# Kernel optimization log

Measured on AMD Instinct MI355X. Metric: run time of the kernel, lower is better.

Reference implementation:

```python
import jax, jax.numpy as jnp
import numpy as np

N = 50000   # nodes
E = 400000  # edges
R = 35      # num_relations
B = 12      # num_bases
C = 128     # hidden_conv_dim (heads=1)
T = 4       # node types: load, gen, load_gen, ext
HL = 38     # hidden_lin_dim
OUT = 2


def setup_inputs() -> dict:
    key = jax.random.key(0)
    ks = jax.random.split(key, 24)
    s = 0.1  # param scale
    inp = {
        'x': jax.random.normal(ks[0], (N, 2), jnp.float32),
        'edge_index': jax.random.randint(ks[1], (2, E), 0, N, jnp.int32),
        'edge_type': jax.random.randint(ks[2], (E,), 0, R, jnp.int32),
        'edge_attr': jax.random.normal(ks[3], (E, 2), jnp.float32),
        'node_type': jax.random.randint(ks[4], (N,), 0, T, jnp.int32),
        'basis': jax.random.normal(ks[5], (B, 2, C), jnp.float32) * s,
        'att_rel': jax.random.normal(ks[6], (R, B), jnp.float32) * s,
        'q_att': jax.random.normal(ks[7], (C, 1), jnp.float32) * s,
        'k_att': jax.random.normal(ks[8], (C, 1), jnp.float32) * s,
        'e_att': jax.random.normal(ks[9], (C, 1), jnp.float32) * s,
        'lin_edge_W': jax.random.normal(ks[10], (2, C), jnp.float32) * s,
        'conv_bias': jax.random.normal(ks[11], (C,), jnp.float32) * s,
        'lin0_W': jax.random.normal(ks[12], (T, C, HL), jnp.float32) * s,
        'lin0_b': jax.random.normal(ks[13], (T, HL), jnp.float32) * s,
        'lin1_W': jax.random.normal(ks[14], (T, HL, HL), jnp.float32) * s,
        'lin1_b': jax.random.normal(ks[15], (T, HL), jnp.float32) * s,
        'lin2_W': jax.random.normal(ks[16], (T, HL, HL), jnp.float32) * s,
        'lin2_b': jax.random.normal(ks[17], (T, HL), jnp.float32) * s,
        'fin_W': jax.random.normal(ks[18], (T, HL, OUT), jnp.float32) * s,
        'fin_b': jax.random.normal(ks[19], (T, OUT), jnp.float32) * s,
    }
    return inp


def _segment_softmax(alpha, dst, n):
    # PyG softmax: max is detached, eps=1e-16 on the denominator
    amax = jax.lax.stop_gradient(jax.ops.segment_max(alpha, dst, num_segments=n))
    ex = jnp.exp(alpha - amax[dst])
    den = jax.ops.segment_sum(ex, dst, num_segments=n) + 1e-16
    return ex / den[dst]


def _per_type_linear(xv, W, b, t):
    # apply node-type-specific Linear: [N,d] x [T,d,h] -> pick row type
    y = jnp.einsum('nd,tdh->nth', xv, W)              # [N,T,h]
    y = jnp.take_along_axis(y, t[:, None, None], axis=1)[:, 0]
    return y + b[t]


def reference(x, edge_index, edge_type, edge_attr, node_type,
              basis, att_rel, q_att, k_att, e_att, lin_edge_W, conv_bias,
              lin0_W, lin0_b, lin1_W, lin1_b, lin2_W, lin2_b, fin_W, fin_b):
    n = x.shape[0]
    src, dst = edge_index[0], edge_index[1]
    # RGATConv with basis decomposition: per-relation weight [R, in=2, C]
    w = jnp.einsum('rb,bio->rio', att_rel, basis)
    w_e = w[edge_type]                                 # [E,2,C] edge gather
    out_i = jnp.einsum('ei,eic->ec', x[dst], w_e)      # [E,C]
    out_j = jnp.einsum('ei,eic->ec', x[src], w_e)      # [E,C]
    ke = (edge_attr @ lin_edge_W) @ e_att              # [E,1]
    alpha = out_i @ q_att + out_j @ k_att + ke         # additive self-attention
    alpha = jax.nn.leaky_relu(alpha, 0.2)
    alpha = _segment_softmax(alpha, dst, n)            # across-relation segment softmax
    msg = alpha * out_j                                # heads=1 -> [E,C]
    agg = jax.ops.segment_sum(msg, dst, num_segments=n) + conv_bias
    h = jax.nn.leaky_relu(agg, 0.2)                    # forward activation (dropout: eval)
    t = node_type
    h = _per_type_linear(jax.nn.relu(h), lin0_W, lin0_b, t)
    h = _per_type_linear(jax.nn.relu(h), lin1_W, lin1_b, t)
    h = _per_type_linear(jax.nn.relu(h), lin2_W, lin2_b, t)
    out = _per_type_linear(h, fin_W, fin_b, t)         # [N,2]
    # load nodes (type 0): second output passes through abs
    load_out = jnp.concatenate([out[:, :1], jnp.abs(out[:, 1:2])], axis=1)
    return jnp.where((t == 0)[:, None], load_out, out)
```

## Files before the change

kernel.cpp:

```cpp
#include <hip/hip_runtime.h>
#include <math.h>

#define N_NODES 50000
#define N_EDGES 400000
#define R_REL   35
#define B_BASES 12
#define C_DIM   128
#define HL_DIM  38
#define RI2     70
#define NP      50304
#define NB_HIST 196
#define NBUCK   786
#define EPB     2048
#define CAP     704

#define OFF_WT     0
#define OFF_WQ     8960
#define OFF_WK     9030
#define OFF_LE     9100
#define OFF_META   9104
#define OFF_HBLK   9120
#define OFF_BBASE  9904
#define OFF_PERM   10688
#define OFF_INV    60688
#define OFF_ECUR   110992
#define OFF_EREC   111780

#define CH    0
#define ST    3584
#define HH    8344
#define Y2T   11608
#define SM_DINV 16536
#define SM_CB   16600
#define SM_B0   16728
#define SM_B1   16766
#define SM_B2   16804
#define SM_FW   16844
#define SM_FB   16920
#define LDS_FLOATS 16928

__global__ __launch_bounds__(256) void k_init(const int* __restrict__ node_type,
                                              const float* __restrict__ basis,
                                              const float* __restrict__ att_rel,
                                              float* __restrict__ ws) {
    int b = blockIdx.x, tid = threadIdx.x;
    if (b < NB_HIST) {
        __shared__ int lh[4];
        if (tid < 4) lh[tid] = 0;
        __syncthreads();
        int i = b * 256 + tid;
        if (i < N_NODES) atomicAdd(&lh[node_type[i]], 1);
        __syncthreads();
        if (tid < 4) ((int*)(ws + OFF_HBLK))[b * 4 + tid] = lh[tid];
    } else if (b < NB_HIST + 35) {
        int idx = (b - NB_HIST) * 256 + tid;
        if (idx < RI2 * C_DIM) {
            int c  = idx & (C_DIM - 1);
            int ri = idx >> 7;
            int r = ri >> 1, ii = ri & 1;
            float acc = 0.f;
            #pragma unroll
            for (int bb = 0; bb < B_BASES; ++bb)
                acc += att_rel[r * B_BASES + bb] * basis[(bb * 2 + ii) * C_DIM + c];
            ws[OFF_WT + idx] = acc;
        }
    } else {
        for (int i = tid; i < NBUCK; i += 256) ((int*)(ws + OFF_ECUR))[i] = 0;
    }
}

__global__ __launch_bounds__(256) void k_scanproj(const float* __restrict__ q_att,
                                                  const float* __restrict__ k_att,
                                                  const float* __restrict__ e_att,
                                                  const float* __restrict__ lin_edge_W,
                                                  float* __restrict__ ws) {
    int b = blockIdx.x, tid = threadIdx.x;
    int lane = tid & 63, wv = tid >> 6;
    if (b == 0) {
        __shared__ int lh[NB_HIST * 4];
        __shared__ int basel[4];
        const int* hblk = (const int*)(ws + OFF_HBLK);
        for (int i = tid; i < NB_HIST * 4; i += 256) lh[i] = hblk[i];
        __syncthreads();
        __shared__ int tot[4];
        if (tid < 4) {
            int run = 0;
            for (int bb = 0; bb < NB_HIST; ++bb) {
                int v = lh[bb * 4 + tid];
                lh[bb * 4 + tid] = run;
                run += v;
            }
            tot[tid] = run;
        }
        __syncthreads();
        if (tid == 0) {
            int* meta = (int*)(ws + OFF_META);
            int t0 = tot[0], t1 = tot[1], t2 = tot[2], t3 = tot[3];
            int b1 = ((t0 + 63) >> 6) << 6;
            int b2 = b1 + (((t1 + 63) >> 6) << 6);
            int b3 = b2 + (((t2 + 63) >> 6) << 6);
            meta[0] = t0; meta[1] = t1; meta[2] = t2; meta[3] = t3;
            meta[4] = 0;  meta[5] = b1; meta[6] = b2; meta[7] = b3;
            basel[0] = 0; basel[1] = b1; basel[2] = b2; basel[3] = b3;
        }
        __syncthreads();
        for (int i = tid; i < NB_HIST * 4; i += 256)
            ((int*)(ws + OFF_BBASE))[i] = basel[i & 3] + lh[i];
    } else {
        int u = (b - 1) * 4 + wv;
        if (u < RI2) {
            const float* wr = ws + OFF_WT + u * C_DIM;
            float w1 = wr[lane], w2 = wr[64 + lane];
            float aq = w1 * q_att[lane] + w2 * q_att[64 + lane];
            float ak = w1 * k_att[lane] + w2 * k_att[64 + lane];
            #pragma unroll
            for (int off = 32; off; off >>= 1) {
                aq += __shfl_xor(aq, off, 64);
                ak += __shfl_xor(ak, off, 64);
            }
            if (lane == 0) { ws[OFF_WQ + u] = aq; ws[OFF_WK + u] = ak; }
        } else if (u < 72) {
            int j = u - RI2;
            const float* er = lin_edge_W + j * C_DIM;
            float a = er[lane] * e_att[lane] + er[64 + lane] * e_att[64 + lane];
            #pragma unroll
            for (int off = 32; off; off >>= 1) a += __shfl_xor(a, off, 64);
            if (lane == 0) ws[OFF_LE + j] = a;
        }
    }
}

__global__ __launch_bounds__(256) void k_perm(const int* __restrict__ node_type,
                                              float* __restrict__ ws) {
    __shared__ int wcnt[4][4];
    int tid = threadIdx.x;
    int lane = tid & 63, wv = tid >> 6;
    int n = blockIdx.x * 256 + tid;
    bool active = n < N_NODES;
    int ty = active ? node_type[n] : -1;
    int myrank = 0;
    #pragma unroll
    for (int t = 0; t < 4; ++t) {
        unsigned long long m = __ballot(ty == t);
        if (lane == 0) wcnt[wv][t] = __popcll(m);
        if (ty == t) myrank = __popcll(m & ((1ULL << lane) - 1ULL));
    }
    __syncthreads();
    if (active) {
        int pre = 0;
        for (int w2 = 0; w2 < wv; ++w2) pre += wcnt[w2][ty];
        int p = ((const int*)(ws + OFF_BBASE))[blockIdx.x * 4 + ty] + pre + myrank;
        ((int*)(ws + OFF_PERM))[n] = p;
        ((int*)(ws + OFF_INV))[p] = n;
    }
}

__global__ __launch_bounds__(256) void k_escatter(const float* __restrict__ x,
                                                  const int* __restrict__ edge_index,
                                                  const int* __restrict__ edge_type,
                                                  const float* __restrict__ edge_attr,
                                                  float* __restrict__ ws) {
    __shared__ int hist[NBUCK];
    __shared__ int sbase[NBUCK];
    __shared__ float swq[RI2], swk[RI2], sle[2];
    int tid = threadIdx.x;
    for (int i = tid; i < NBUCK; i += 256) hist[i] = 0;
    if (tid < RI2) { swq[tid] = ws[OFF_WQ + tid]; swk[tid] = ws[OFF_WK + tid]; }
    if (tid < 2) sle[tid] = ws[OFF_LE + tid];
    __syncthreads();

    const int* perm = (const int*)(ws + OFF_PERM);
    int base = blockIdx.x * EPB;
    int   rb[8], rm[8];
    float rex[8], rsx[8], rsy[8];
    #pragma unroll
    for (int k = 0; k < 8; ++k) {
        int e = base + k * 256 + tid;
        rb[k] = -1;
        if (e < N_EDGES) {
            int src = edge_index[e];
            int dst = edge_index[N_EDGES + e];
            int r   = edge_type[e];
            int p   = perm[dst];
            float2 ea = *(const float2*)(edge_attr + 2 * e);
            float2 xs = *(const float2*)(x + 2 * src);
            float2 xd = *(const float2*)(x + 2 * dst);
            float alpha = xd.x * swq[2 * r] + xd.y * swq[2 * r + 1]
                        + xs.x * swk[2 * r] + xs.y * swk[2 * r + 1]
                        + ea.x * sle[0]     + ea.y * sle[1];
            alpha = alpha > 0.f ? alpha : 0.2f * alpha;
            float ex = __expf(alpha);
            rb[k]  = p >> 6;
            rm[k]  = (r << 6) | (p & 63);
            rex[k] = ex;
            rsx[k] = ex * xs.x;
            rsy[k] = ex * xs.y;
            atomicAdd(&hist[rb[k]], 1);
        }
    }
    __syncthreads();
    int* gcur = (int*)(ws + OFF_ECUR);
    for (int i = tid; i < NBUCK; i += 256) {
        int c = hist[i];
        sbase[i] = (c > 0) ? atomicAdd(&gcur[i], c) : 0;
    }
    __syncthreads();
    float4* rec = (float4*)(ws + OFF_EREC);
    #pragma unroll
    for (int k = 0; k < 8; ++k) {
        if (rb[k] >= 0) {
            int slot = atomicAdd(&sbase[rb[k]], 1);
            rec[(size_t)rb[k] * CAP + slot] =
                make_float4(__int_as_float(rm[k]), rex[k], rsx[k], rsy[k]);
        }
    }
}

__global__ __launch_bounds__(256) void k_node(
        const float* __restrict__ ws, const float* __restrict__ conv_bias,
        const float* __restrict__ lin0_W, const float* __restrict__ lin0_b,
        const float* __restrict__ lin1_W, const float* __restrict__ lin1_b,
        const float* __restrict__ lin2_W, const float* __restrict__ lin2_b,
        const float* __restrict__ fin_W,  const float* __restrict__ fin_b,
        float* __restrict__ out) {
    __shared__ float L[LDS_FLOATS];
    int tid  = threadIdx.x;
    int lane = tid & 63;
    int wv   = tid >> 6;
    int p0   = blockIdx.x * 64;

    const int* meta = (const int*)(ws + OFF_META);
    int b1 = meta[5], b2 = meta[6], b3 = meta[7];
    int t  = (p0 >= b1) + (p0 >= b2) + (p0 >= b3);
    int bp = meta[4 + t];
    int cnt = meta[t];

    for (int i = tid; i < RI2 * 68; i += 256) L[ST + i] = 0.f;
    if (tid < 64) L[SM_DINV + tid] = 0.f;
    if (tid < 128) L[SM_CB + tid] = conv_bias[tid];
    if (tid >= 64 && tid < 256) {
        int i = tid - 64;
        if      (i < 38)  L[SM_B0 + i]        = lin0_b[t * HL_DIM + i];
        else if (i < 76)  L[SM_B1 + i - 38]   = lin1_b[t * HL_DIM + i - 38];
        else if (i < 114) L[SM_B2 + i - 76]   = lin2_b[t * HL_DIM + i - 76];
        else if (i < 190) L[SM_FW + i - 114]  = fin_W[t * 76 + i - 114];
        else              L[SM_FB + i - 190]  = fin_b[t * 2 + i - 190];
    }
    const float* wT_g = ws + OFF_WT;
    for (int i4 = tid; i4 < 448; i4 += 256) {
        float4 v = ((const float4*)wT_g)[i4];
        *(float4*)&L[CH + i4 * 4] = v;
    }
    __syncthreads();

    {
        int ecnt = ((const int*)(ws + OFF_ECUR))[blockIdx.x];
        const float4* rec = (const float4*)(ws + OFF_EREC) + (size_t)blockIdx.x * CAP;
        for (int i = tid; i < ecnt; i += 256) {
            float4 v = rec[i];
            int m = __float_as_int(v.x);
            int n = m & 63, r = m >> 6;
            atomicAdd(&L[ST + (2 * r) * 68 + n],     v.z);
            atomicAdd(&L[ST + (2 * r + 1) * 68 + n], v.w);
            atomicAdd(&L[SM_DINV + n],               v.y);
        }
    }
    __syncthreads();
    if (tid < 64) L[SM_DINV + tid] = 1.0f / (L[SM_DINV + tid] + 1e-16f);

    int ng = lane & 15, cg_ = lane >> 4;
    int c0 = wv * 32 + cg_ * 8;
    float acc[32];
    #pragma unroll
    for (int i = 0; i < 32; ++i) acc[i] = 0.f;
    int cur = 0;
    for (int q = 0; q < 5; ++q) {
        float4 pf0, pf1;
        if (q < 4) {
            const float4* src = (const float4*)(wT_g + (q + 1) * 1792);
            pf0 = src[tid];
            if (tid < 192) pf1 = src[tid + 256];
        }
        const float* wb = &L[CH + cur * 1792];
        #pragma unroll
        for (int kk = 0; kk < 14; ++kk) {
            float4 a4 = *(const float4*)&L[ST + (q * 14 + kk) * 68 + ng * 4];
            float4 wa = *(const float4*)&wb[kk * 128 + c0];
            float4 wc = *(const float4*)&wb[kk * 128 + c0 + 4];
            float a_[4] = {a4.x, a4.y, a4.z, a4.w};
            float w_[8] = {wa.x, wa.y, wa.z, wa.w, wc.x, wc.y, wc.z, wc.w};
            #pragma unroll
            for (int ni = 0; ni < 4; ++ni)
                #pragma unroll
                for (int ci = 0; ci < 8; ++ci)
                    acc[ni * 8 + ci] += a_[ni] * w_[ci];
        }
        if (q < 4) {
            float* dstb = &L[CH + (cur ^ 1) * 1792];
            *(float4*)&dstb[tid * 4] = pf0;
            if (tid < 192) *(float4*)&dstb[(tid + 256) * 4] = pf1;
        }
        cur ^= 1;
        __syncthreads();
    }

    {
        float4 dv = *(const float4*)&L[SM_DINV + ng * 4];
        float d_[4] = {dv.x, dv.y, dv.z, dv.w};
        #pragma unroll
        for (int ci = 0; ci < 8; ++ci) {
            float cb = L[SM_CB + c0 + ci];
            float4 hv;
            float h0 = acc[0 * 8 + ci] * d_[0] + cb;
            float h1 = acc[1 * 8 + ci] * d_[1] + cb;
            float h2 = acc[2 * 8 + ci] * d_[2] + cb;
            float h3 = acc[3 * 8 + ci] * d_[3] + cb;
            hv.x = h0 > 0.f ? h0 : 0.f;
            hv.y = h1 > 0.f ? h1 : 0.f;
            hv.z = h2 > 0.f ? h2 : 0.f;
            hv.w = h3 > 0.f ? h3 : 0.f;
            *(float4*)&L[HH + (c0 + ci) * 64 + ng * 4] = hv;
        }
    }
    const float* W0g = lin0_W + t * C_DIM * HL_DIM;
    for (int i = tid; i < 608; i += 256) {
        int cc = i / 38, j = i - cc * 38;
        L[CH + cc * 40 + j] = W0g[i];
    }
    __syncthreads();

    int jg = lane >> 4;
    int j0 = wv * 16 + jg * 4;
    float acc2[16];
    #pragma unroll
    for (int i = 0; i < 16; ++i) acc2[i] = 0.f;
    int cur2 = 0;
    for (int q = 0; q < 8; ++q) {
        float pa, pb, pc;
        if (q < 7) {
            const float* src = W0g + (q + 1) * 608;
            pa = src[tid];
            if (tid < 608 - 256) pb = src[tid + 256];
            if (tid < 608 - 512) pc = src[tid + 512];
        }
        const float* wb = &L[CH + cur2 * 1792];
        #pragma unroll
        for (int kk = 0; kk < 16; ++kk) {
            int c = q * 16 + kk;
            float4 a4 = *(const float4*)&L[HH + c * 64 + ng * 4];
            float4 w4 = *(const float4*)&wb[kk * 40 + j0];
            float a_[4] = {a4.x, a4.y, a4.z, a4.w};
            float w_[4] = {w4.x, w4.y, w4.z, w4.w};
            #pragma unroll
            for (int ni = 0; ni < 4; ++ni)
                #pragma unroll
                for (int ji = 0; ji < 4; ++ji)
                    acc2[ni * 4 + ji] += a_[ni] * w_[ji];
        }
        if (q < 7) {
            float* dstb = &L[CH + (cur2 ^ 1) * 1792];
            int i = tid, cc = i / 38, j = i - cc * 38;
            dstb[cc * 40 + j] = pa;
            if (tid < 608 - 256) { i = tid + 256; cc = i / 38; j = i - cc * 38; dstb[cc * 40 + j] = pb; }
            if (tid < 608 - 512) { i = tid + 512; cc = i / 38; j = i - cc * 38; dstb[cc * 40 + j] = pc; }
        }
        cur2 ^= 1;
        __syncthreads();
    }
    #pragma unroll
    for (int ji = 0; ji < 4; ++ji) {
        int j = j0 + ji;
        float b = (j < 38) ? L[SM_B0 + j] : 0.f;
        float4 yv;
        float y0 = acc2[0 * 4 + ji] + b;
        float y1 = acc2[1 * 4 + ji] + b;
        float y2 = acc2[2 * 4 + ji] + b;
        float y3 = acc2[3 * 4 + ji] + b;
        yv.x = y0 > 0.f ? y0 : 0.f;
        yv.y = y1 > 0.f ? y1 : 0.f;
        yv.z = y2 > 0.f ? y2 : 0.f;
        yv.w = y3 > 0.f ? y3 : 0.f;
        *(float4*)&L[ST + j * 68 + ng * 4] = yv;
    }
    {
        const float* W1g = lin1_W + t * HL_DIM * HL_DIM;
        const float* W2g = lin2_W + t * HL_DIM * HL_DIM;
        for (int i = tid; i < 1444; i += 256) {
            int cc = i / 38, j = i - cc * 38;
            L[CH + cc * 40 + j] = W1g[i];
            L[CH + 1520 + cc * 40 + j] = W2g[i];
        }
    }
    __syncthreads();

    float acc3[16];
    #pragma unroll
    for (int i = 0; i < 16; ++i) acc3[i] = 0.f;
    #pragma unroll 2
    for (int kk = 0; kk < 38; ++kk) {
        float4 a4 = *(const float4*)&L[ST + kk * 68 + ng * 4];
        float4 w4 = *(const float4*)&L[CH + kk * 40 + j0];
        float a_[4] = {a4.x, a4.y, a4.z, a4.w};
        float w_[4] = {w4.x, w4.y, w4.z, w4.w};
        #pragma unroll
        for (int ni = 0; ni < 4; ++ni)
            #pragma unroll
            for (int ji = 0; ji < 4; ++ji)
                acc3[ni * 4 + ji] += a_[ni] * w_[ji];
    }
    __syncthreads();
    #pragma unroll
    for (int ji = 0; ji < 4; ++ji) {
        int j = j0 + ji;
        float b = (j < 38) ? L[SM_B1 + j] : 0.f;
        float4 yv;
        float y0 = acc3[0 * 4 + ji] + b;
        float y1 = acc3[1 * 4 + ji] + b;
        float y2 = acc3[2 * 4 + ji] + b;
        float y3 = acc3[3 * 4 + ji] + b;
        yv.x = y0 > 0.f ? y0 : 0.f;
        yv.y = y1 > 0.f ? y1 : 0.f;
        yv.z = y2 > 0.f ? y2 : 0.f;
        yv.w = y3 > 0.f ? y3 : 0.f;
        *(float4*)&L[HH + j * 68 + ng * 4] = yv;
    }
    __syncthreads();

    float acc4[16];
    #pragma unroll
    for (int i = 0; i < 16; ++i) acc4[i] = 0.f;
    #pragma unroll 2
    for (int kk = 0; kk < 38; ++kk) {
        float4 a4 = *(const float4*)&L[HH + kk * 68 + ng * 4];
        float4 w4 = *(const float4*)&L[CH + 1520 + kk * 40 + j0];
        float a_[4] = {a4.x, a4.y, a4.z, a4.w};
        float w_[4] = {w4.x, w4.y, w4.z, w4.w};
        #pragma unroll
        for (int ni = 0; ni < 4; ++ni)
            #pragma unroll
            for (int ji = 0; ji < 4; ++ji)
                acc4[ni * 4 + ji] += a_[ni] * w_[ji];
    }
    #pragma unroll
    for (int ji = 0; ji < 4; ++ji) {
        int j = j0 + ji;
        float b = (j < 38) ? L[SM_B2 + j] : 0.f;
        float4 yv;
        yv.x = acc4[0 * 4 + ji] + b;
        yv.y = acc4[1 * 4 + ji] + b;
        yv.z = acc4[2 * 4 + ji] + b;
        yv.w = acc4[3 * 4 + ji] + b;
        *(float4*)&L[Y2T + j * 68 + ng * 4] = yv;
    }
    __syncthreads();

    if (tid < 64) {
        int p = p0 + tid;
        bool valid = (p - bp) < cnt;
        float o0 = L[SM_FB], o1 = L[SM_FB + 1];
        for (int jj = 0; jj < 38; ++jj) {
            float v = L[Y2T + jj * 68 + tid];
            float2 f = *(const float2*)&L[SM_FW + jj * 2];
            o0 += v * f.x;
            o1 += v * f.y;
        }
        if (t == 0) o1 = fabsf(o1);
        if (valid) {
            int orig = ((const int*)(ws + OFF_INV))[p];
            ((float2*)out)[orig] = make_float2(o0, o1);
        }
    }
}

extern "C" void kernel_launch(void* const* d_in, const int* in_sizes, int n_in,
                              void* d_out, int out_size, void* d_ws, size_t ws_size,
                              hipStream_t stream) {
    const float* x          = (const float*)d_in[0];
    const int*   edge_index = (const int*)  d_in[1];
    const int*   edge_type  = (const int*)  d_in[2];
    const float* edge_attr  = (const float*)d_in[3];
    const int*   node_type  = (const int*)  d_in[4];
    const float* basis      = (const float*)d_in[5];
    const float* att_rel    = (const float*)d_in[6];
    const float* q_att      = (const float*)d_in[7];
    const float* k_att      = (const float*)d_in[8];
    const float* e_att      = (const float*)d_in[9];
    const float* lin_edge_W = (const float*)d_in[10];
    const float* conv_bias  = (const float*)d_in[11];
    const float* lin0_W     = (const float*)d_in[12];
    const float* lin0_b     = (const float*)d_in[13];
    const float* lin1_W     = (const float*)d_in[14];
    const float* lin1_b     = (const float*)d_in[15];
    const float* lin2_W     = (const float*)d_in[16];
    const float* lin2_b     = (const float*)d_in[17];
    const float* fin_W      = (const float*)d_in[18];
    const float* fin_b      = (const float*)d_in[19];

    float* ws  = (float*)d_ws;
    float* out = (float*)d_out;

    k_init    <<<NB_HIST + 35 + 1, 256, 0, stream>>>(node_type, basis, att_rel, ws);
    k_scanproj<<<19, 256, 0, stream>>>(q_att, k_att, e_att, lin_edge_W, ws);
    k_perm    <<<NB_HIST, 256, 0, stream>>>(node_type, ws);
    k_escatter<<<NB_HIST, 256, 0, stream>>>(x, edge_index, edge_type, edge_attr, ws);
    k_node    <<<NBUCK, 256, 0, stream>>>(ws, conv_bias,
                                          lin0_W, lin0_b, lin1_W, lin1_b,
                                          lin2_W, lin2_b, fin_W, fin_b, out);
}
```

Baseline: 175.9 us.

## Shrink k_node LDS footprint by aliasing buffers to raise occupancy

Reorganizes the k_node shared-memory layout so the hidden, layer-output and weight buffers alias one another, cutting LDS from about 66KB to about 39KB per block, and adds a launch bound of 4 blocks. The lin0 weight staging drops double buffering for simple 32-row chunks with barriers. Warp 3, whose output columns only cover padding past the 38 hidden units, now skips the MLP matmuls, and biases are read straight from global memory. Higher occupancy should hide latency better, at the cost of more barriers and losing the prefetch overlap in the lin0 loop.

```diff
diff --git a/kernel.cpp b/kernel.cpp
--- a/kernel.cpp
+++ b/kernel.cpp
@@ -28,16 +28,17 @@
 
 #define CH    0
 #define ST    3584
-#define HH    8344
-#define Y2T   11608
-#define SM_DINV 16536
-#define SM_CB   16600
-#define SM_B0   16728
-#define SM_B1   16766
-#define SM_B2   16804
-#define SM_FW   16844
-#define SM_FB   16920
-#define LDS_FLOATS 16928
+#define HH    0
+#define Y0T   0
+#define W1S   3264
+#define W2S   4784
+#define Y1T   6304
+#define Y2T   0
+#define W0Q   8344
+#define SM_DINV 9624
+#define SM_FW   9688
+#define SM_FB   9764
+#define LDS_FLOATS 9766
 
 __global__ __launch_bounds__(256) void k_init(const int* __restrict__ node_type,
                                               const float* __restrict__ basis,
@@ -216,7 +217,7 @@
     }
 }
 
-__global__ __launch_bounds__(256) void k_node(
+__global__ __launch_bounds__(256, 4) void k_node(
         const float* __restrict__ ws, const float* __restrict__ conv_bias,
         const float* __restrict__ lin0_W, const float* __restrict__ lin0_b,
         const float* __restrict__ lin1_W, const float* __restrict__ lin1_b,
@@ -237,14 +238,10 @@
 
     for (int i = tid; i < RI2 * 68; i += 256) L[ST + i] = 0.f;
     if (tid < 64) L[SM_DINV + tid] = 0.f;
-    if (tid < 128) L[SM_CB + tid] = conv_bias[tid];
-    if (tid >= 64 && tid < 256) {
+    if (tid >= 64 && tid < 142) {
         int i = tid - 64;
-        if      (i < 38)  L[SM_B0 + i]        = lin0_b[t * HL_DIM + i];
-        else if (i < 76)  L[SM_B1 + i - 38]   = lin1_b[t * HL_DIM + i - 38];
-        else if (i < 114) L[SM_B2 + i - 76]   = lin2_b[t * HL_DIM + i - 76];
-        else if (i < 190) L[SM_FW + i - 114]  = fin_W[t * 76 + i - 114];
-        else              L[SM_FB + i - 190]  = fin_b[t * 2 + i - 190];
+        if (i < 76) L[SM_FW + i] = fin_W[t * 76 + i];
+        else        L[SM_FB + i - 76] = fin_b[t * 2 + i - 76];
     }
     const float* wT_g = ws + OFF_WT;
     for (int i4 = tid; i4 < 448; i4 += 256) {
@@ -309,7 +306,7 @@
         float d_[4] = {dv.x, dv.y, dv.z, dv.w};
         #pragma unroll
         for (int ci = 0; ci < 8; ++ci) {
-            float cb = L[SM_CB + c0 + ci];
+            float cb = conv_bias[c0 + ci];
             float4 hv;
             float h0 = acc[0 * 8 + ci] * d_[0] + cb;
             float h1 = acc[1 * 8 + ci] * d_[1] + cb;
@@ -322,73 +319,61 @@
             *(float4*)&L[HH + (c0 + ci) * 64 + ng * 4] = hv;
         }
     }
+    __syncthreads();
+
     const float* W0g = lin0_W + t * C_DIM * HL_DIM;
-    for (int i = tid; i < 608; i += 256) {
-        int cc = i / 38, j = i - cc * 38;
-        L[CH + cc * 40 + j] = W0g[i];
-    }
-    __syncthreads();
-
     int jg = lane >> 4;
     int j0 = wv * 16 + jg * 4;
     float acc2[16];
     #pragma unroll
     for (int i = 0; i < 16; ++i) acc2[i] = 0.f;
-    int cur2 = 0;
-    for (int q = 0; q < 8; ++q) {
-        float pa, pb, pc;
-        if (q < 7) {
-            const float* src = W0g + (q + 1) * 608;
-            pa = src[tid];
-            if (tid < 608 - 256) pb = src[tid + 256];
-            if (tid < 608 - 512) pc = src[tid + 512];
-        }
-        const float* wb = &L[CH + cur2 * 1792];
-        #pragma unroll
-        for (int kk = 0; kk < 16; ++kk) {
-            int c = q * 16 + kk;
-            float4 a4 = *(const float4*)&L[HH + c * 64 + ng * 4];
-            float4 w4 = *(const float4*)&wb[kk * 40 + j0];
-            float a_[4] = {a4.x, a4.y, a4.z, a4.w};
-            float w_[4] = {w4.x, w4.y, w4.z, w4.w};
-            #pragma unroll
-            for (int ni = 0; ni < 4; ++ni)
+    for (int q = 0; q < 4; ++q) {
+        for (int i = tid; i < 1216; i += 256) {
+            int cc = i / 38, j = i - cc * 38;
+            L[W0Q + cc * 40 + j] = W0g[q * 1216 + i];
+        }
+        __syncthreads();
+        if (wv < 3) {
+            #pragma unroll 4
+            for (int kk = 0; kk < 32; ++kk) {
+                int c = q * 32 + kk;
+                float4 a4 = *(const float4*)&L[HH + c * 64 + ng * 4];
+                float4 w4 = *(const float4*)&L[W0Q + kk * 40 + j0];
+                float a_[4] = {a4.x, a4.y, a4.z, a4.w};
+                float w_[4] = {w4.x, w4.y, w4.z, w4.w};
                 #pragma unroll
-                for (int ji = 0; ji < 4; ++ji)
-                    acc2[ni * 4 + ji] += a_[ni] * w_[ji];
-        }
-        if (q < 7) {
-            float* dstb = &L[CH + (cur2 ^ 1) * 1792];
-            int i = tid, cc = i / 38, j = i - cc * 38;
-            dstb[cc * 40 + j] = pa;
-            if (tid < 608 - 256) { i = tid + 256; cc = i / 38; j = i - cc * 38; dstb[cc * 40 + j] = pb; }
-            if (tid < 608 - 512) { i = tid + 512; cc = i / 38; j = i - cc * 38; dstb[cc * 40 + j] = pc; }
-        }
-        cur2 ^= 1;
-        __syncthreads();
-    }
-    #pragma unroll
-    for (int ji = 0; ji < 4; ++ji) {
-        int j = j0 + ji;
-        float b = (j < 38) ? L[SM_B0 + j] : 0.f;
-        float4 yv;
-        float y0 = acc2[0 * 4 + ji] + b;
-        float y1 = acc2[1 * 4 + ji] + b;
-        float y2 = acc2[2 * 4 + ji] + b;
-        float y3 = acc2[3 * 4 + ji] + b;
-        yv.x = y0 > 0.f ? y0 : 0.f;
-        yv.y = y1 > 0.f ? y1 : 0.f;
-        yv.z = y2 > 0.f ? y2 : 0.f;
-        yv.w = y3 > 0.f ? y3 : 0.f;
-        *(float4*)&L[ST + j * 68 + ng * 4] = yv;
+                for (int ni = 0; ni < 4; ++ni)
+                    #pragma unroll
+                    for (int ji = 0; ji < 4; ++ji)
+                        acc2[ni * 4 + ji] += a_[ni] * w_[ji];
+            }
+        }
+        __syncthreads();
+    }
+    if (wv < 3) {
+        #pragma unroll
+        for (int ji = 0; ji < 4; ++ji) {
+            int j = j0 + ji;
+            float b = (j < HL_DIM) ? lin0_b[t * HL_DIM + j] : 0.f;
+            float4 yv;
+            float y0 = acc2[0 * 4 + ji] + b;
+            float y1 = acc2[1 * 4 + ji] + b;
+            float y2 = acc2[2 * 4 + ji] + b;
+            float y3 = acc2[3 * 4 + ji] + b;
+            yv.x = y0 > 0.f ? y0 : 0.f;
+            yv.y = y1 > 0.f ? y1 : 0.f;
+            yv.z = y2 > 0.f ? y2 : 0.f;
+            yv.w = y3 > 0.f ? y3 : 0.f;
+            *(float4*)&L[Y0T + j * 68 + ng * 4] = yv;
+        }
     }
     {
         const float* W1g = lin1_W + t * HL_DIM * HL_DIM;
         const float* W2g = lin2_W + t * HL_DIM * HL_DIM;
         for (int i = tid; i < 1444; i += 256) {
             int cc = i / 38, j = i - cc * 38;
-            L[CH + cc * 40 + j] = W1g[i];
-            L[CH + 1520 + cc * 40 + j] = W2g[i];
+            L[W1S + cc * 40 + j] = W1g[i];
+            L[W2S + cc * 40 + j] = W2g[i];
         }
     }
     __syncthreads();
@@ -396,61 +381,64 @@
     float acc3[16];
     #pragma unroll
     for (int i = 0; i < 16; ++i) acc3[i] = 0.f;
-    #pragma unroll 2
-    for (int kk = 0; kk < 38; ++kk) {
-        float4 a4 = *(const float4*)&L[ST + kk * 68 + ng * 4];
-        float4 w4 = *(const float4*)&L[CH + kk * 40 + j0];
-        float a_[4] = {a4.x, a4.y, a4.z, a4.w};
-        float w_[4] = {w4.x, w4.y, w4.z, w4.w};
-        #pragma unroll
-        for (int ni = 0; ni < 4; ++ni)
-            #pragma unroll
-            for (int ji = 0; ji < 4; ++ji)
-                acc3[ni * 4 + ji] += a_[ni] * w_[ji];
-    }
-    __syncthreads();
-    #pragma unroll
-    for (int ji = 0; ji < 4; ++ji) {
-        int j = j0 + ji;
-        float b = (j < 38) ? L[SM_B1 + j] : 0.f;
-        float4 yv;
-        float y0 = acc3[0 * 4 + ji] + b;
-        float y1 = acc3[1 * 4 + ji] + b;
-        float y2 = acc3[2 * 4 + ji] + b;
-        float y3 = acc3[3 * 4 + ji] + b;
-        yv.x = y0 > 0.f ? y0 : 0.f;
-        yv.y = y1 > 0.f ? y1 : 0.f;
-        yv.z = y2 > 0.f ? y2 : 0.f;
-        yv.w = y3 > 0.f ? y3 : 0.f;
-        *(float4*)&L[HH + j * 68 + ng * 4] = yv;
-    }
-    __syncthreads();
-
-    float acc4[16];
-    #pragma unroll
-    for (int i = 0; i < 16; ++i) acc4[i] = 0.f;
-    #pragma unroll 2
-    for (int kk = 0; kk < 38; ++kk) {
-        float4 a4 = *(const float4*)&L[HH + kk * 68 + ng * 4];
-        float4 w4 = *(const float4*)&L[CH + 1520 + kk * 40 + j0];
-        float a_[4] = {a4.x, a4.y, a4.z, a4.w};
-        float w_[4] = {w4.x, w4.y, w4.z, w4.w};
-        #pragma unroll
-        for (int ni = 0; ni < 4; ++ni)
-            #pragma unroll
-            for (int ji = 0; ji < 4; ++ji)
-                acc4[ni * 4 + ji] += a_[ni] * w_[ji];
-    }
-    #pragma unroll
-    for (int ji = 0; ji < 4; ++ji) {
-        int j = j0 + ji;
-        float b = (j < 38) ? L[SM_B2 + j] : 0.f;
-        float4 yv;
-        yv.x = acc4[0 * 4 + ji] + b;
-        yv.y = acc4[1 * 4 + ji] + b;
-        yv.z = acc4[2 * 4 + ji] + b;
-        yv.w = acc4[3 * 4 + ji] + b;
-        *(float4*)&L[Y2T + j * 68 + ng * 4] = yv;
+    if (wv < 3) {
+        #pragma unroll 2
+        for (int kk = 0; kk < HL_DIM; ++kk) {
+            float4 a4 = *(const float4*)&L[Y0T + kk * 68 + ng * 4];
+            float4 w4 = *(const float4*)&L[W1S + kk * 40 + j0];
+            float a_[4] = {a4.x, a4.y, a4.z, a4.w};
+            float w_[4] = {w4.x, w4.y, w4.z, w4.w};
+            #pragma unroll
+            for (int ni = 0; ni < 4; ++ni)
+                #pragma unroll
+                for (int ji = 0; ji < 4; ++ji)
+                    acc3[ni * 4 + ji] += a_[ni] * w_[ji];
+        }
+        #pragma unroll
+        for (int ji = 0; ji < 4; ++ji) {
+            int j = j0 + ji;
+            float b = (j < HL_DIM) ? lin1_b[t * HL_DIM + j] : 0.f;
+            float4 yv;
+            float y0 = acc3[0 * 4 + ji] + b;
+            float y1 = acc3[1 * 4 + ji] + b;
+            float y2 = acc3[2 * 4 + ji] + b;
+            float y3 = acc3[3 * 4 + ji] + b;
+            yv.x = y0 > 0.f ? y0 : 0.f;
+            yv.y = y1 > 0.f ? y1 : 0.f;
+            yv.z = y2 > 0.f ? y2 : 0.f;
+            yv.w = y3 > 0.f ? y3 : 0.f;
+            *(float4*)&L[Y1T + j * 68 + ng * 4] = yv;
+        }
+    }
+    __syncthreads();
+
+    if (wv < 3) {
+        float acc4[16];
+        #pragma unroll
+        for (int i = 0; i < 16; ++i) acc4[i] = 0.f;
+        #pragma unroll 2
+        for (int kk = 0; kk < HL_DIM; ++kk) {
+            float4 a4 = *(const float4*)&L[Y1T + kk * 68 + ng * 4];
+            float4 w4 = *(const float4*)&L[W2S + kk * 40 + j0];
+            float a_[4] = {a4.x, a4.y, a4.z, a4.w};
+            float w_[4] = {w4.x, w4.y, w4.z, w4.w};
+            #pragma unroll
+            for (int ni = 0; ni < 4; ++ni)
+                #pragma unroll
+                for (int ji = 0; ji < 4; ++ji)
+                    acc4[ni * 4 + ji] += a_[ni] * w_[ji];
+        }
+        #pragma unroll
+        for (int ji = 0; ji < 4; ++ji) {
+            int j = j0 + ji;
+            float b = (j < HL_DIM) ? lin2_b[t * HL_DIM + j] : 0.f;
+            float4 yv;
+            yv.x = acc4[0 * 4 + ji] + b;
+            yv.y = acc4[1 * 4 + ji] + b;
+            yv.z = acc4[2 * 4 + ji] + b;
+            yv.w = acc4[3 * 4 + ji] + b;
+            *(float4*)&L[Y2T + j * 68 + ng * 4] = yv;
+        }
     }
     __syncthreads();
 
@@ -458,7 +446,7 @@
         int p = p0 + tid;
         bool valid = (p - bp) < cnt;
         float o0 = L[SM_FB], o1 = L[SM_FB + 1];
-        for (int jj = 0; jj < 38; ++jj) {
+        for (int jj = 0; jj < HL_DIM; ++jj) {
             float v = L[Y2T + jj * 68 + tid];
             float2 f = *(const float2*)&L[SM_FW + jj * 2];
             o0 += v * f.x;
```

Result: slower. 253.2 us (+43.9%).
